# Kernel tuning notes

Hardware: AMD Instinct MI355X
Metric: run time of the kernel (lower is better)

Reference implementation:

```python
import jax, jax.numpy as jnp
import numpy as np

# ---- static config ----
G = 4          # num graphs
NG = 512       # nodes per graph
N = G * NG     # total nodes
E = 32768      # num edges
IN_DIM = 128
HID = 32
HEADS = 4
HC = HID * HEADS  # 128
OUT_DIM = 32
N_LAYERS = 2
GRID = 500
Q = 20
NEG_SLOPE = 0.2
QUANTILES = jnp.asarray(np.linspace(0.0, 1.0, Q), jnp.float32)  # [Q]


def setup_inputs() -> dict:
    key = jax.random.key(0)
    ks = jax.random.split(key, 32)
    inp = {}
    inp['x'] = jax.random.normal(ks[0], (N, IN_DIM), jnp.float32)
    inp['edge_index'] = jax.random.randint(ks[1], (2, E), 0, N).astype(jnp.int64)
    inp['batch'] = (jnp.arange(N) // NG).astype(jnp.int64)
    # GATConv params (2 layers, both 128 -> 4 heads x 32, concat)
    for l, (kin,) in enumerate([(IN_DIM,), (HC,)]):
        s = 1.0 / np.sqrt(kin)
        inp[f'W{l}'] = jax.random.normal(ks[2 + 4 * l], (kin, HC), jnp.float32) * s
        inp[f'as{l}'] = jax.random.normal(ks[3 + 4 * l], (HEADS, HID), jnp.float32) * s
        inp[f'ad{l}'] = jax.random.normal(ks[4 + 4 * l], (HEADS, HID), jnp.float32) * s
        inp[f'b{l}'] = jnp.zeros((HC,), jnp.float32)
    for l in range(N_LAYERS + 1):
        inp[f'lpW{l}'] = jax.random.normal(ks[10 + 2 * l], (HC, OUT_DIM), jnp.float32) * (1.0 / np.sqrt(HC))
        inp[f'lpb{l}'] = jnp.zeros((OUT_DIM,), jnp.float32)
    for l in range(N_LAYERS + 1):
        inp[f'kW{l}'] = jax.random.normal(ks[16 + 2 * l], (HC * Q, OUT_DIM), jnp.float32) * (1.0 / np.sqrt(HC * Q))
        inp[f'kb{l}'] = jnp.zeros((OUT_DIM,), jnp.float32)
    inp['pool_w'] = jnp.ones((2,), jnp.float32) / 2.0
    inp['beta'] = jax.random.normal(ks[22], (OUT_DIM,), jnp.float32)
    inp['h0'] = jax.random.normal(ks[23], (1,), jnp.float32)
    return inp


def _gat_layer(x, src, dst, W, a_src, a_dst, bias):
    # PyG GATConv (concat=True, add_self_loops=True, negative_slope=0.2), eval mode
    n = x.shape[0]
    xh = (x @ W).reshape(n, HEADS, HID)              # [N,H,C]
    loop = jnp.arange(n)
    s = jnp.concatenate([src, loop])                 # [E+N]
    d = jnp.concatenate([dst, loop])
    al_s = jnp.einsum('nhc,hc->nh', xh, a_src)       # [N,H]
    al_d = jnp.einsum('nhc,hc->nh', xh, a_dst)
    e = jax.nn.leaky_relu(al_s[s] + al_d[d], NEG_SLOPE)   # [E+N,H]
    e_max = jax.ops.segment_max(e, d, num_segments=n)     # stable softmax per dst
    e = jnp.exp(e - e_max[d])
    denom = jax.ops.segment_sum(e, d, num_segments=n)
    alpha = e / (denom[d] + 1e-16)                   # [E+N,H]
    out = jax.ops.segment_sum(alpha[:, :, None] * xh[s], d, num_segments=n)
    return out.reshape(n, HC) + bias


def _kde_per_graph(xg):
    # xg: [Ng, D] -> [D*Q] soft-quantile features via grid KDE
    n = xg.shape[0]
    mn = xg.min(axis=0) - 1e-6                       # [D]
    mx = xg.max(axis=0) + 1e-6
    grid = jnp.linspace(0.0, 1.0, GRID)[:, None] * (mx - mn) + mn   # [Gp,D]
    std = xg.std(axis=0) + 1e-8 / 3
    h = 1.06 * std * float(n) ** (-0.2)              # [D]
    u = (grid[:, None, :] - xg[None, :, :]) / h      # [Gp,Ng,D]  (dominant tensor)
    kern = jnp.exp(-0.5 * u * u) / (h * np.sqrt(2.0 * np.pi))
    density = kern.mean(axis=1)                      # [Gp,D]
    cdf = jnp.cumsum(density, axis=0)
    cdf = cdf / jnp.clip(cdf[-1:], 1e-8)
    dist = jnp.abs(cdf[:, :, None] - QUANTILES)      # [Gp,D,Q]
    w = jax.nn.sigmoid(-100.0 * dist)
    w = w / (w.sum(axis=0, keepdims=True) + 1e-8)
    qv = (grid[:, :, None] * w).sum(axis=0)          # [D,Q]
    return qv.reshape(-1)


def _readout(cur, lpW, lpb, kW, kb, pool_w):
    xr = cur.reshape(G, NG, -1)
    pooled = jnp.stack([xr.mean(axis=1), xr.max(axis=1)], axis=0)   # [2,G,D]
    wp = (pooled * pool_w[:, None, None]).sum(axis=0)               # [G,D]
    h = wp @ lpW + lpb                                              # [G,out]
    kf = jax.vmap(_kde_per_graph)(xr)                               # [G,D*Q]
    return h, kf @ kW + kb


def reference(x, edge_index, batch, W0, as0, ad0, b0, W1, as1, ad1, b1,
              lpW0, lpb0, lpW1, lpb1, lpW2, lpb2,
              kW0, kb0, kW1, kb1, kW2, kb2, pool_w, beta, h0):
    src, dst = edge_index[0], edge_index[1]
    convs = [(W0, as0, ad0, b0), (W1, as1, ad1, b1)]
    lps = [(lpW0, lpb0), (lpW1, lpb1), (lpW2, lpb2)]
    kps = [(kW0, kb0), (kW1, kb1), (kW2, kb2)]
    cur = x
    h_list, kde_list = [], []
    for i in range(N_LAYERS):
        h, kp = _readout(cur, lps[i][0], lps[i][1], kps[i][0], kps[i][1], pool_w)
        h_list.append(h); kde_list.append(kp)
        cur = _gat_layer(cur, src, dst, *convs[i])
        if i != N_LAYERS - 1:
            cur = jax.nn.relu(cur)
    h, kp = _readout(cur, lps[-1][0], lps[-1][1], kps[-1][0], kps[-1][1], pool_w)
    h_list.append(h); kde_list.append(kp)
    main_out = jnp.stack(h_list).mean(axis=0)        # [G,out]
    kde_out = jnp.stack(kde_list).mean(axis=0)
    risk = (main_out + kde_out) @ beta + h0          # [G]
    return risk
```

## Files before the change

### kernel.cpp

```cpp
#include <hip/hip_runtime.h>
#include <math.h>

#define GNUM 4
#define NG 512
#define NN 2048
#define EE 32768
#define HC 128
#define HEADS 4
#define HID 32
#define GRID_PTS 500
#define QN 20
#define ODIM 32
#define MAXE 160

#define LOG2E 1.44269504088896340736f
#define NEG_HALF_LOG2E -0.72134752044448170368f
#define N_POW_M02 0.2871745887492588f
#define SIG_K 144.269504089f

__device__ __forceinline__ float fexp2(float x){ return __builtin_amdgcn_exp2f(x); }
__device__ __forceinline__ float frcp(float x){ return __builtin_amdgcn_rcpf(x); }

struct SmemKDE {
  __align__(16) float2 xs[NG];
  float4 wred4[8];
  float sc[4];
  float wsum[8], woff[9];
  float redw[QN][8], redg[QN][8];
  float qs[QN];
};
struct SmemXW  { float rows[4][HC]; int cnt[4]; };
struct SmemGat {
  int   ssrc[4][MAXE];
  float sexp[4][MAXE][HEADS];
};
union Smem { SmemKDE kde; SmemXW xw; SmemGat gat; };

__device__ void kde_phase(Smem& sm, const float* __restrict__ cur, int do_relu, int trans,
        const float* __restrict__ kW, const float* __restrict__ kb, float* __restrict__ kacc,
        const float* __restrict__ lpW, const float* __restrict__ lpb,
        const float* __restrict__ poolw, float* __restrict__ macc){
  int b = blockIdx.x;
  int g = b >> 7, d = b & 127;
  int t = threadIdx.x;
  int lane = t & 63, wave = t >> 6;
  float v, v2;
  if (trans){
    float2 vv = ((const float2*)cur)[(size_t)d*NN + g*NG + t];
    v = vv.x; v2 = vv.y;
  } else {
    v = cur[((size_t)g*NG + t)*HC + d];
    v2 = v*v;
  }
  if (do_relu){ v = fmaxf(v, 0.f); v2 = v*v; }
  if (!trans) sm.kde.xs[t] = make_float2(v, v2);
  float mn=v, mx=v, smv=v, sq=v2;
  #pragma unroll
  for (int m=32; m>0; m>>=1){
    mn = fminf(mn, __shfl_xor(mn, m, 64));
    mx = fmaxf(mx, __shfl_xor(mx, m, 64));
    smv += __shfl_xor(smv, m, 64);
    sq += __shfl_xor(sq, m, 64);
  }
  if (lane==0) sm.kde.wred4[wave] = make_float4(mn,mx,smv,sq);
  __syncthreads();
  if (t==0){
    float4 r = sm.kde.wred4[0];
    #pragma unroll
    for (int i=1;i<8;++i){
      float4 bb = sm.kde.wred4[i];
      r.x = fminf(r.x,bb.x); r.y = fmaxf(r.y,bb.y); r.z += bb.z; r.w += bb.w;
    }
    float mean = r.z * (1.f/NG);
    float var  = fmaxf(r.w*(1.f/NG) - mean*mean, 0.f);
    float sd   = sqrtf(var) + (1e-8f/3.f);
    float h    = 1.06f * sd * N_POW_M02;
    float lo = r.x - 1e-6f, hi = r.y + 1e-6f;
    sm.kde.sc[0] = lo;
    sm.kde.sc[1] = (hi-lo)*(1.f/(GRID_PTS-1));
    sm.kde.sc[2] = NEG_HALF_LOG2E/(h*h);
    sm.kde.sc[3] = poolw[0]*mean + poolw[1]*r.y;
  }
  __syncthreads();
  float lo = sm.kde.sc[0], st = sm.kde.sc[1], kk = sm.kde.sc[2];
  float gv = lo + st*(float)t;
  float acc = 0.f;
  if (t < GRID_PTS){
    float c0 = kk*gv*gv, c1 = -2.f*kk*gv;
    const float4* p4 = trans ? ((const float4*)cur) + (((size_t)d*NN + g*NG) >> 1)
                             : (const float4*)sm.kde.xs;
    #pragma unroll 4
    for (int i=0;i<NG/2;++i){
      float4 s2 = p4[i];
      acc += fexp2(fmaf(kk, s2.y, fmaf(c1, s2.x, c0)));
      acc += fexp2(fmaf(kk, s2.w, fmaf(c1, s2.z, c0)));
    }
  }
  float sv = acc;
  #pragma unroll
  for (int off=1; off<64; off<<=1){
    float n = __shfl_up(sv, off, 64);
    if (lane >= off) sv += n;
  }
  if (lane==63) sm.kde.wsum[wave] = sv;
  __syncthreads();
  if (t==0){
    float r2 = 0.f;
    #pragma unroll
    for (int i=0;i<8;++i){ sm.kde.woff[i]=r2; r2+=sm.kde.wsum[i]; }
    sm.kde.woff[8]=r2;
  }
  if (t < QN*8){ ((float*)sm.kde.redw)[t]=0.f; ((float*)sm.kde.redg)[t]=0.f; }
  __syncthreads();
  float invt = 1.f/fmaxf(sm.kde.woff[8], 1e-8f);
  float c = (sv + sm.kde.woff[wave]) * invt;
  float cw0 = __shfl(c, 0, 64), cw1 = __shfl(c, 63, 64);
  int qlo = max(0, (int)ceilf((cw0 - 0.17f)*(float)(QN-1)));
  int qhi = min(QN-1, (int)floorf((cw1 + 0.17f)*(float)(QN-1)));
  for (int q=qlo; q<=qhi; ++q){
    float w = 0.f;
    if (t < GRID_PTS){
      float dist = fabsf(c - (float)q*(1.f/(QN-1)));
      w = frcp(1.f + fexp2(SIG_K*dist));
    }
    float gw = gv*w;
    #pragma unroll
    for (int m=32;m>0;m>>=1){
      w  += __shfl_xor(w,  m, 64);
      gw += __shfl_xor(gw, m, 64);
    }
    if (lane==0){ sm.kde.redw[q][wave]=w; sm.kde.redg[q][wave]=gw; }
  }
  __syncthreads();
  if (t < QN){
    float sw=0.f, sgw=0.f;
    #pragma unroll
    for (int i=0;i<8;++i){ sw+=sm.kde.redw[t][i]; sgw+=sm.kde.redg[t][i]; }
    sm.kde.qs[t] = sgw / (sw + 1e-8f);
  }
  __syncthreads();
  if (t < ODIM){
    float a = 0.f;
    const float* kwb = kW + (size_t)d*QN*ODIM + t;
    #pragma unroll
    for (int q=0;q<QN;++q) a += sm.kde.qs[q]*kwb[q*ODIM];
    if (d==0) a += kb[t];
    kacc[(size_t)d*128 + g*ODIM + t] = a;
    float bb = sm.kde.sc[3]*lpW[d*ODIM + t];
    if (d==0) bb += lpb[t];
    macc[(size_t)d*128 + g*ODIM + t] = bb;
  }
  __syncthreads();
}

__device__ float gather_core(Smem& sm, int d, int sub, int tl,
        const int* __restrict__ csr, const int* __restrict__ deg,
        const float* __restrict__ als, const float* __restrict__ ald,
        const float* __restrict__ xh, const float* __restrict__ bias){
  int dg = deg[d];
  int E = dg + 1;
  const int* base = csr + d*MAXE;
  float a0 = ald[d*4+0], a1 = ald[d*4+1], a2 = ald[d*4+2], a3 = ald[d*4+3];
  for (int i=tl; i<E; i+=128){
    int s = (i < dg) ? base[i] : d;
    sm.gat.ssrc[sub][i] = s;
    float e0 = als[s*4+0]+a0, e1 = als[s*4+1]+a1, e2 = als[s*4+2]+a2, e3 = als[s*4+3]+a3;
    e0 = (e0>=0.f)? e0 : 0.2f*e0;
    e1 = (e1>=0.f)? e1 : 0.2f*e1;
    e2 = (e2>=0.f)? e2 : 0.2f*e2;
    e3 = (e3>=0.f)? e3 : 0.2f*e3;
    sm.gat.sexp[sub][i][0]=e0; sm.gat.sexp[sub][i][1]=e1;
    sm.gat.sexp[sub][i][2]=e2; sm.gat.sexp[sub][i][3]=e3;
  }
  __syncthreads();
  int h = tl >> 5, l32 = tl & 31;
  float mx = -INFINITY;
  for (int i=l32; i<E; i+=32) mx = fmaxf(mx, sm.gat.sexp[sub][i][h]);
  #pragma unroll
  for (int m=16; m>0; m>>=1) mx = fmaxf(mx, __shfl_xor(mx, m, 32));
  float sdn = 0.f;
  for (int i=l32; i<E; i+=32){
    float ev = fexp2(LOG2E*(sm.gat.sexp[sub][i][h] - mx));
    sm.gat.sexp[sub][i][h] = ev;
    sdn += ev;
  }
  #pragma unroll
  for (int m=16; m>0; m>>=1) sdn += __shfl_xor(sdn, m, 32);
  float fac = 1.f/(sdn + 1e-16f);
  float acc = bias[tl];
  for (int i=0;i<E;++i)
    acc += sm.gat.sexp[sub][i][h]*fac * xh[(size_t)sm.gat.ssrc[sub][i]*HC + tl];
  __syncthreads();
  return acc;
}

__device__ void xw_emit(Smem& sm, int sub, int j, int n,
        const float* __restrict__ W, const float* __restrict__ as_, const float* __restrict__ ad_,
        float* __restrict__ xh, float* __restrict__ als, float* __restrict__ ald){
  float acc = 0.f;
  #pragma unroll 8
  for (int c2=0;c2<HC;++c2)
    acc += sm.xw.rows[sub][c2]*W[(size_t)c2*HC + j];
  xh[(size_t)n*HC + j] = acc;
  int h = j >> 5, cc = j & 31;
  float ps = acc*as_[h*HID+cc], pd = acc*ad_[h*HID+cc];
  #pragma unroll
  for (int m=16;m>0;m>>=1){
    ps += __shfl_xor(ps, m, 32);
    pd += __shfl_xor(pd, m, 32);
  }
  if (cc==0){ als[n*HEADS+h]=ps; ald[n*HEADS+h]=pd; }
}

__device__ void write_transposed(Smem& sm, int t, int n0, float* __restrict__ curT){
  if (t < HC){
    float v0 = sm.xw.rows[0][t], v1 = sm.xw.rows[1][t];
    float v2 = sm.xw.rows[2][t], v3 = sm.xw.rows[3][t];
    float4* p = (float4*)(curT + (((size_t)t*NN + n0) << 1));
    p[0] = make_float4(v0, v0*v0, v1, v1*v1);
    p[1] = make_float4(v2, v2*v2, v3, v3*v3);
  }
}

__global__ __launch_bounds__(512) void k_L0(const float* __restrict__ x,
        const float* __restrict__ kW, const float* __restrict__ kb, float* __restrict__ kacc,
        const float* __restrict__ lpW, const float* __restrict__ lpb,
        const float* __restrict__ poolw, float* __restrict__ macc,
        const float* __restrict__ W, const float* __restrict__ as_, const float* __restrict__ ad_,
        float* __restrict__ xh, float* __restrict__ als, float* __restrict__ ald,
        const int* __restrict__ src, const int* __restrict__ dst,
        int* __restrict__ deg, int* __restrict__ csr){
  __shared__ Smem sm;
  int t = threadIdx.x;
  if (blockIdx.x < 512){
    kde_phase(sm, x, 0, 0, kW, kb, kacc, lpW, lpb, poolw, macc);
  } else {
    int b2 = blockIdx.x - 512;
    int sub = t >> 7, j = t & 127;
    int n = b2*4 + sub;
    if (t < 4) sm.xw.cnt[t] = 0;
    sm.xw.rows[sub][j] = x[(size_t)n*HC + j];
    __syncthreads();
    int base4 = b2*4;
    for (int e = t; e < EE; e += 512){
      int dd = dst[e];
      unsigned r = (unsigned)(dd - base4);
      if (r < 4u){
        int p = atomicAdd(&sm.xw.cnt[r], 1);
        if (p < MAXE) csr[dd*MAXE + p] = src[e];
      }
    }
    xw_emit(sm, sub, j, n, W, as_, ad_, xh, als, ald);
    __syncthreads();
    if (t < 4) deg[base4 + t] = min(sm.xw.cnt[t], MAXE-1);
  }
}

__global__ __launch_bounds__(512) void k_G0(const int* __restrict__ csr, const int* __restrict__ deg,
        const float* __restrict__ als_in, const float* __restrict__ ald_in,
        const float* __restrict__ xh_in, const float* __restrict__ bias,
        float* __restrict__ cur1T,
        const float* __restrict__ W1, const float* __restrict__ as1, const float* __restrict__ ad1,
        float* __restrict__ xh2, float* __restrict__ als2, float* __restrict__ ald2){
  __shared__ Smem sm;
  int t = threadIdx.x;
  int sub = t >> 7, tl = t & 127;
  int d = blockIdx.x*4 + sub;
  float acc = gather_core(sm, d, sub, tl, csr, deg, als_in, ald_in, xh_in, bias);
  sm.xw.rows[sub][tl] = fmaxf(acc, 0.f);
  __syncthreads();
  write_transposed(sm, t, blockIdx.x*4, cur1T);
  xw_emit(sm, sub, tl, d, W1, as1, ad1, xh2, als2, ald2);
}

__global__ __launch_bounds__(512) void k_L1(const float* __restrict__ cur1T,
        const float* __restrict__ kW, const float* __restrict__ kb, float* __restrict__ kacc,
        const float* __restrict__ lpW, const float* __restrict__ lpb,
        const float* __restrict__ poolw, float* __restrict__ macc,
        const int* __restrict__ csr, const int* __restrict__ deg,
        const float* __restrict__ als2, const float* __restrict__ ald2,
        const float* __restrict__ xh2, const float* __restrict__ bias,
        float* __restrict__ cur2T){
  __shared__ Smem sm;
  int t = threadIdx.x;
  if (blockIdx.x < 512){
    kde_phase(sm, cur1T, 0, 1, kW, kb, kacc, lpW, lpb, poolw, macc);
  } else {
    int b2 = blockIdx.x - 512;
    int sub = t >> 7, tl = t & 127;
    int d = b2*4 + sub;
    float acc = gather_core(sm, d, sub, tl, csr, deg, als2, ald2, xh2, bias);
    sm.xw.rows[sub][tl] = acc;
    __syncthreads();
    write_transposed(sm, t, b2*4, cur2T);
  }
}

__global__ __launch_bounds__(512) void k_L2(const float* __restrict__ cur2T,
        const float* __restrict__ kW, const float* __restrict__ kb, float* __restrict__ kacc,
        const float* __restrict__ lpW, const float* __restrict__ lpb,
        const float* __restrict__ poolw, float* __restrict__ macc){
  __shared__ Smem sm;
  kde_phase(sm, cur2T, 0, 1, kW, kb, kacc, lpW, lpb, poolw, macc);
}

__global__ __launch_bounds__(384) void k_final(const float* __restrict__ mpart, const float* __restrict__ kpart,
                        const float* __restrict__ beta, const float* __restrict__ h0,
                        float* __restrict__ out){
  int t = threadIdx.x;
  __shared__ float sdm[384];
  int l = t >> 7, tt = t & 127;
  const float* mrow = mpart + (size_t)l*16384 + tt;
  const float* krow = kpart + (size_t)l*16384 + tt;
  float s = 0.f;
  #pragma unroll 8
  for (int d2=0; d2<128; ++d2) s += mrow[(size_t)d2*128] + krow[(size_t)d2*128];
  sdm[t] = s;
  __syncthreads();
  if (t < 128){
    int g = t >> 5, o = t & 31;
    float s3 = (sdm[t] + sdm[t+128] + sdm[t+256]) * (1.f/3.f) * beta[o];
    #pragma unroll
    for (int m=16; m>0; m>>=1) s3 += __shfl_xor(s3, m, 32);
    if (o == 0) out[g] = s3 + h0[0];
  }
}

extern "C" void kernel_launch(void* const* d_in, const int* in_sizes, int n_in,
                              void* d_out, int out_size, void* d_ws, size_t ws_size,
                              hipStream_t stream) {
  (void)in_sizes; (void)n_in; (void)out_size; (void)ws_size;
  const float* x    = (const float*)d_in[0];
  const int*   ei   = (const int*)d_in[1];
  const int*   srcp = ei;
  const int*   dstp = ei + EE;
  const float* W[2]   = {(const float*)d_in[3], (const float*)d_in[7]};
  const float* As[2]  = {(const float*)d_in[4], (const float*)d_in[8]};
  const float* Ad[2]  = {(const float*)d_in[5], (const float*)d_in[9]};
  const float* Bi[2]  = {(const float*)d_in[6], (const float*)d_in[10]};
  const float* lpW[3] = {(const float*)d_in[11], (const float*)d_in[13], (const float*)d_in[15]};
  const float* lpb[3] = {(const float*)d_in[12], (const float*)d_in[14], (const float*)d_in[16]};
  const float* kW[3]  = {(const float*)d_in[17], (const float*)d_in[19], (const float*)d_in[21]};
  const float* kb[3]  = {(const float*)d_in[18], (const float*)d_in[20], (const float*)d_in[22]};
  const float* poolw  = (const float*)d_in[23];
  const float* beta   = (const float*)d_in[24];
  const float* h0     = (const float*)d_in[25];
  float* out = (float*)d_out;

  float* ws = (float*)d_ws;
  float* cur1T = ws;
  float* cur2T = cur1T + 524288;
  float* xh    = cur2T + 524288;
  float* xh2   = xh + 262144;
  float* als   = xh2 + 262144;
  float* ald   = als + 8192;
  float* als2  = ald + 8192;
  float* ald2  = als2 + 8192;
  float* mpart = ald2 + 8192;
  float* kpart = mpart + 49152;
  int*   deg   = (int*)(kpart + 49152);
  int*   csr   = deg + 2048;

  k_L0<<<1024, 512, 0, stream>>>(x, kW[0], kb[0], kpart, lpW[0], lpb[0], poolw, mpart,
                                 W[0], As[0], Ad[0], xh, als, ald,
                                 srcp, dstp, deg, csr);
  k_G0<<<512, 512, 0, stream>>>(csr, deg, als, ald, xh, Bi[0], cur1T,
                                W[1], As[1], Ad[1], xh2, als2, ald2);
  k_L1<<<1024, 512, 0, stream>>>(cur1T, kW[1], kb[1], kpart+16384, lpW[1], lpb[1], poolw, mpart+16384,
                                 csr, deg, als2, ald2, xh2, Bi[1], cur2T);
  k_L2<<<512, 512, 0, stream>>>(cur2T, kW[2], kb[2], kpart+32768, lpW[2], lpb[2], poolw, mpart+32768);
  k_final<<<1, 384, 0, stream>>>(mpart, kpart, beta, h0, out);
}
```

Measured before the change: 208.6 us.

## Merge all phases into one cooperative persistent kernel with grid syncs

Replaces the five separate kernel launches with a single cooperative kernel of 512 blocks that runs every phase and separates them with grid-wide barriers. Each block now does both the KDE readout work and the GAT work of a former dual-role launch, and the order alternates by block parity to balance load. This removes launch gaps and tail effects between kernels. The cost is fewer blocks per phase (512 instead of 1024), extra grid-sync latency, and a requirement that all blocks stay co-resident. If the cooperative launch fails, the code falls back to five separate launches.

```diff
diff --git a/kernel.cpp b/kernel.cpp
--- a/kernel.cpp
+++ b/kernel.cpp
@@ -1,5 +1,8 @@
 #include <hip/hip_runtime.h>
+#include <hip/hip_cooperative_groups.h>
 #include <math.h>
+
+namespace cg = cooperative_groups;
 
 #define GNUM 4
 #define NG 512
@@ -36,11 +39,21 @@
 };
 union Smem { SmemKDE kde; SmemXW xw; SmemGat gat; };
 
-__device__ void kde_phase(Smem& sm, const float* __restrict__ cur, int do_relu, int trans,
+struct Params {
+  const float *x; const int *src, *dst;
+  const float *W0,*as0,*ad0,*b0, *W1,*as1,*ad1,*b1;
+  const float *lpW0,*lpb0,*lpW1,*lpb1,*lpW2,*lpb2;
+  const float *kW0,*kb0,*kW1,*kb1,*kW2,*kb2;
+  const float *poolw,*beta,*h0;
+  float *cur1T,*cur2T,*xh,*xh2,*als,*ald,*als2,*ald2,*mpart,*kpart;
+  int *deg,*csr;
+  float *out;
+};
+
+__device__ void kde_phase(Smem& sm, const float* __restrict__ cur, int do_relu, int trans, int b,
         const float* __restrict__ kW, const float* __restrict__ kb, float* __restrict__ kacc,
         const float* __restrict__ lpW, const float* __restrict__ lpb,
         const float* __restrict__ poolw, float* __restrict__ macc){
-  int b = blockIdx.x;
   int g = b >> 7, d = b & 127;
   int t = threadIdx.x;
   int lane = t & 63, wave = t >> 6;
@@ -222,109 +235,112 @@
   }
 }
 
-__global__ __launch_bounds__(512) void k_L0(const float* __restrict__ x,
-        const float* __restrict__ kW, const float* __restrict__ kb, float* __restrict__ kacc,
-        const float* __restrict__ lpW, const float* __restrict__ lpb,
-        const float* __restrict__ poolw, float* __restrict__ macc,
-        const float* __restrict__ W, const float* __restrict__ as_, const float* __restrict__ ad_,
-        float* __restrict__ xh, float* __restrict__ als, float* __restrict__ ald,
-        const int* __restrict__ src, const int* __restrict__ dst,
-        int* __restrict__ deg, int* __restrict__ csr){
-  __shared__ Smem sm;
-  int t = threadIdx.x;
-  if (blockIdx.x < 512){
-    kde_phase(sm, x, 0, 0, kW, kb, kacc, lpW, lpb, poolw, macc);
+__device__ void xw0_task(Smem& sm, const Params& p, int bid, int t){
+  int sub = t >> 7, j = t & 127;
+  int n = bid*4 + sub;
+  if (t < 4) sm.xw.cnt[t] = 0;
+  sm.xw.rows[sub][j] = p.x[(size_t)n*HC + j];
+  __syncthreads();
+  int base4 = bid*4;
+  for (int e = t; e < EE; e += 512){
+    int dd = p.dst[e];
+    unsigned r = (unsigned)(dd - base4);
+    if (r < 4u){
+      int pp = atomicAdd(&sm.xw.cnt[r], 1);
+      if (pp < MAXE) p.csr[dd*MAXE + pp] = p.src[e];
+    }
+  }
+  xw_emit(sm, sub, j, n, p.W0, p.as0, p.ad0, p.xh, p.als, p.ald);
+  __syncthreads();
+  if (t < 4) p.deg[base4 + t] = min(sm.xw.cnt[t], MAXE-1);
+  __syncthreads();
+}
+
+__device__ void gather1_task(Smem& sm, const Params& p, int bid, int t){
+  int sub = t >> 7, tl = t & 127;
+  int d = bid*4 + sub;
+  float acc = gather_core(sm, d, sub, tl, p.csr, p.deg, p.als2, p.ald2, p.xh2, p.b1);
+  sm.xw.rows[sub][tl] = acc;
+  __syncthreads();
+  write_transposed(sm, t, bid*4, p.cur2T);
+  __syncthreads();
+}
+
+__device__ void phaseA(Smem& sm, const Params& p, int bid, int t){
+  if (bid & 1){
+    xw0_task(sm, p, bid, t);
+    kde_phase(sm, p.x, 0, 0, bid, p.kW0, p.kb0, p.kpart, p.lpW0, p.lpb0, p.poolw, p.mpart);
   } else {
-    int b2 = blockIdx.x - 512;
-    int sub = t >> 7, j = t & 127;
-    int n = b2*4 + sub;
-    if (t < 4) sm.xw.cnt[t] = 0;
-    sm.xw.rows[sub][j] = x[(size_t)n*HC + j];
-    __syncthreads();
-    int base4 = b2*4;
-    for (int e = t; e < EE; e += 512){
-      int dd = dst[e];
-      unsigned r = (unsigned)(dd - base4);
-      if (r < 4u){
-        int p = atomicAdd(&sm.xw.cnt[r], 1);
-        if (p < MAXE) csr[dd*MAXE + p] = src[e];
-      }
-    }
-    xw_emit(sm, sub, j, n, W, as_, ad_, xh, als, ald);
-    __syncthreads();
-    if (t < 4) deg[base4 + t] = min(sm.xw.cnt[t], MAXE-1);
-  }
-}
-
-__global__ __launch_bounds__(512) void k_G0(const int* __restrict__ csr, const int* __restrict__ deg,
-        const float* __restrict__ als_in, const float* __restrict__ ald_in,
-        const float* __restrict__ xh_in, const float* __restrict__ bias,
-        float* __restrict__ cur1T,
-        const float* __restrict__ W1, const float* __restrict__ as1, const float* __restrict__ ad1,
-        float* __restrict__ xh2, float* __restrict__ als2, float* __restrict__ ald2){
-  __shared__ Smem sm;
-  int t = threadIdx.x;
+    kde_phase(sm, p.x, 0, 0, bid, p.kW0, p.kb0, p.kpart, p.lpW0, p.lpb0, p.poolw, p.mpart);
+    xw0_task(sm, p, bid, t);
+  }
+}
+
+__device__ void phaseB(Smem& sm, const Params& p, int bid, int t){
   int sub = t >> 7, tl = t & 127;
-  int d = blockIdx.x*4 + sub;
-  float acc = gather_core(sm, d, sub, tl, csr, deg, als_in, ald_in, xh_in, bias);
+  int d = bid*4 + sub;
+  float acc = gather_core(sm, d, sub, tl, p.csr, p.deg, p.als, p.ald, p.xh, p.b0);
   sm.xw.rows[sub][tl] = fmaxf(acc, 0.f);
   __syncthreads();
-  write_transposed(sm, t, blockIdx.x*4, cur1T);
-  xw_emit(sm, sub, tl, d, W1, as1, ad1, xh2, als2, ald2);
-}
-
-__global__ __launch_bounds__(512) void k_L1(const float* __restrict__ cur1T,
-        const float* __restrict__ kW, const float* __restrict__ kb, float* __restrict__ kacc,
-        const float* __restrict__ lpW, const float* __restrict__ lpb,
-        const float* __restrict__ poolw, float* __restrict__ macc,
-        const int* __restrict__ csr, const int* __restrict__ deg,
-        const float* __restrict__ als2, const float* __restrict__ ald2,
-        const float* __restrict__ xh2, const float* __restrict__ bias,
-        float* __restrict__ cur2T){
-  __shared__ Smem sm;
-  int t = threadIdx.x;
-  if (blockIdx.x < 512){
-    kde_phase(sm, cur1T, 0, 1, kW, kb, kacc, lpW, lpb, poolw, macc);
+  write_transposed(sm, t, bid*4, p.cur1T);
+  xw_emit(sm, sub, tl, d, p.W1, p.as1, p.ad1, p.xh2, p.als2, p.ald2);
+}
+
+__device__ void phaseC(Smem& sm, const Params& p, int bid, int t){
+  if (bid & 1){
+    gather1_task(sm, p, bid, t);
+    kde_phase(sm, p.cur1T, 0, 1, bid, p.kW1, p.kb1, p.kpart+16384, p.lpW1, p.lpb1, p.poolw, p.mpart+16384);
   } else {
-    int b2 = blockIdx.x - 512;
-    int sub = t >> 7, tl = t & 127;
-    int d = b2*4 + sub;
-    float acc = gather_core(sm, d, sub, tl, csr, deg, als2, ald2, xh2, bias);
-    sm.xw.rows[sub][tl] = acc;
-    __syncthreads();
-    write_transposed(sm, t, b2*4, cur2T);
-  }
-}
-
-__global__ __launch_bounds__(512) void k_L2(const float* __restrict__ cur2T,
-        const float* __restrict__ kW, const float* __restrict__ kb, float* __restrict__ kacc,
-        const float* __restrict__ lpW, const float* __restrict__ lpb,
-        const float* __restrict__ poolw, float* __restrict__ macc){
-  __shared__ Smem sm;
-  kde_phase(sm, cur2T, 0, 1, kW, kb, kacc, lpW, lpb, poolw, macc);
-}
-
-__global__ __launch_bounds__(384) void k_final(const float* __restrict__ mpart, const float* __restrict__ kpart,
-                        const float* __restrict__ beta, const float* __restrict__ h0,
-                        float* __restrict__ out){
-  int t = threadIdx.x;
-  __shared__ float sdm[384];
-  int l = t >> 7, tt = t & 127;
-  const float* mrow = mpart + (size_t)l*16384 + tt;
-  const float* krow = kpart + (size_t)l*16384 + tt;
-  float s = 0.f;
-  #pragma unroll 8
-  for (int d2=0; d2<128; ++d2) s += mrow[(size_t)d2*128] + krow[(size_t)d2*128];
-  sdm[t] = s;
+    kde_phase(sm, p.cur1T, 0, 1, bid, p.kW1, p.kb1, p.kpart+16384, p.lpW1, p.lpb1, p.poolw, p.mpart+16384);
+    gather1_task(sm, p, bid, t);
+  }
+}
+
+__device__ void phaseD(Smem& sm, const Params& p, int bid, int t){
+  kde_phase(sm, p.cur2T, 0, 1, bid, p.kW2, p.kb2, p.kpart+32768, p.lpW2, p.lpb2, p.poolw, p.mpart+32768);
+}
+
+__device__ void phaseE(Smem& sm, const Params& p, int t){
+  float* sdm = (float*)sm.kde.xs;
+  if (t < 384){
+    int l = t >> 7, tt = t & 127;
+    const float* mrow = p.mpart + (size_t)l*16384 + tt;
+    const float* krow = p.kpart + (size_t)l*16384 + tt;
+    float s = 0.f;
+    #pragma unroll 8
+    for (int d2=0; d2<128; ++d2) s += mrow[(size_t)d2*128] + krow[(size_t)d2*128];
+    sdm[t] = s;
+  }
   __syncthreads();
   if (t < 128){
     int g = t >> 5, o = t & 31;
-    float s3 = (sdm[t] + sdm[t+128] + sdm[t+256]) * (1.f/3.f) * beta[o];
+    float s3 = (sdm[t] + sdm[t+128] + sdm[t+256]) * (1.f/3.f) * p.beta[o];
     #pragma unroll
     for (int m=16; m>0; m>>=1) s3 += __shfl_xor(s3, m, 32);
-    if (o == 0) out[g] = s3 + h0[0];
-  }
-}
+    if (o == 0) p.out[g] = s3 + p.h0[0];
+  }
+}
+
+__global__ __launch_bounds__(512, 4) void k_all(Params p){
+  __shared__ Smem sm;
+  cg::grid_group grid = cg::this_grid();
+  int bid = blockIdx.x, t = threadIdx.x;
+  phaseA(sm, p, bid, t);
+  grid.sync();
+  phaseB(sm, p, bid, t);
+  grid.sync();
+  phaseC(sm, p, bid, t);
+  grid.sync();
+  phaseD(sm, p, bid, t);
+  grid.sync();
+  if (bid == 0) phaseE(sm, p, t);
+}
+
+__global__ __launch_bounds__(512, 4) void k_pA(Params p){ __shared__ Smem sm; phaseA(sm, p, blockIdx.x, threadIdx.x); }
+__global__ __launch_bounds__(512, 4) void k_pB(Params p){ __shared__ Smem sm; phaseB(sm, p, blockIdx.x, threadIdx.x); }
+__global__ __launch_bounds__(512, 4) void k_pC(Params p){ __shared__ Smem sm; phaseC(sm, p, blockIdx.x, threadIdx.x); }
+__global__ __launch_bounds__(512, 4) void k_pD(Params p){ __shared__ Smem sm; phaseD(sm, p, blockIdx.x, threadIdx.x); }
+__global__ __launch_bounds__(512, 4) void k_pE(Params p){ __shared__ Smem sm; if (blockIdx.x == 0) phaseE(sm, p, threadIdx.x); }
 
 extern "C" void kernel_launch(void* const* d_in, const int* in_sizes, int n_in,
                               void* d_out, int out_size, void* d_ws, size_t ws_size,
@@ -332,20 +348,6 @@
   (void)in_sizes; (void)n_in; (void)out_size; (void)ws_size;
   const float* x    = (const float*)d_in[0];
   const int*   ei   = (const int*)d_in[1];
-  const int*   srcp = ei;
-  const int*   dstp = ei + EE;
-  const float* W[2]   = {(const float*)d_in[3], (const float*)d_in[7]};
-  const float* As[2]  = {(const float*)d_in[4], (const float*)d_in[8]};
-  const float* Ad[2]  = {(const float*)d_in[5], (const float*)d_in[9]};
-  const float* Bi[2]  = {(const float*)d_in[6], (const float*)d_in[10]};
-  const float* lpW[3] = {(const float*)d_in[11], (const float*)d_in[13], (const float*)d_in[15]};
-  const float* lpb[3] = {(const float*)d_in[12], (const float*)d_in[14], (const float*)d_in[16]};
-  const float* kW[3]  = {(const float*)d_in[17], (const float*)d_in[19], (const float*)d_in[21]};
-  const float* kb[3]  = {(const float*)d_in[18], (const float*)d_in[20], (const float*)d_in[22]};
-  const float* poolw  = (const float*)d_in[23];
-  const float* beta   = (const float*)d_in[24];
-  const float* h0     = (const float*)d_in[25];
-  float* out = (float*)d_out;
 
   float* ws = (float*)d_ws;
   float* cur1T = ws;
@@ -361,13 +363,34 @@
   int*   deg   = (int*)(kpart + 49152);
   int*   csr   = deg + 2048;
 
-  k_L0<<<1024, 512, 0, stream>>>(x, kW[0], kb[0], kpart, lpW[0], lpb[0], poolw, mpart,
-                                 W[0], As[0], Ad[0], xh, als, ald,
-                                 srcp, dstp, deg, csr);
-  k_G0<<<512, 512, 0, stream>>>(csr, deg, als, ald, xh, Bi[0], cur1T,
-                                W[1], As[1], Ad[1], xh2, als2, ald2);
-  k_L1<<<1024, 512, 0, stream>>>(cur1T, kW[1], kb[1], kpart+16384, lpW[1], lpb[1], poolw, mpart+16384,
-                                 csr, deg, als2, ald2, xh2, Bi[1], cur2T);
-  k_L2<<<512, 512, 0, stream>>>(cur2T, kW[2], kb[2], kpart+32768, lpW[2], lpb[2], poolw, mpart+32768);
-  k_final<<<1, 384, 0, stream>>>(mpart, kpart, beta, h0, out);
-}
+  Params prm;
+  prm.x = x; prm.src = ei; prm.dst = ei + EE;
+  prm.W0 = (const float*)d_in[3];  prm.as0 = (const float*)d_in[4];
+  prm.ad0 = (const float*)d_in[5]; prm.b0  = (const float*)d_in[6];
+  prm.W1 = (const float*)d_in[7];  prm.as1 = (const float*)d_in[8];
+  prm.ad1 = (const float*)d_in[9]; prm.b1  = (const float*)d_in[10];
+  prm.lpW0 = (const float*)d_in[11]; prm.lpb0 = (const float*)d_in[12];
+  prm.lpW1 = (const float*)d_in[13]; prm.lpb1 = (const float*)d_in[14];
+  prm.lpW2 = (const float*)d_in[15]; prm.lpb2 = (const float*)d_in[16];
+  prm.kW0 = (const float*)d_in[17]; prm.kb0 = (const float*)d_in[18];
+  prm.kW1 = (const float*)d_in[19]; prm.kb1 = (const float*)d_in[20];
+  prm.kW2 = (const float*)d_in[21]; prm.kb2 = (const float*)d_in[22];
+  prm.poolw = (const float*)d_in[23];
+  prm.beta  = (const float*)d_in[24];
+  prm.h0    = (const float*)d_in[25];
+  prm.cur1T = cur1T; prm.cur2T = cur2T; prm.xh = xh; prm.xh2 = xh2;
+  prm.als = als; prm.ald = ald; prm.als2 = als2; prm.ald2 = ald2;
+  prm.mpart = mpart; prm.kpart = kpart; prm.deg = deg; prm.csr = csr;
+  prm.out = (float*)d_out;
+
+  void* kargs[] = { (void*)&prm };
+  hipError_t err = hipLaunchCooperativeKernel((const void*)k_all, dim3(512), dim3(512),
+                                              kargs, 0, stream);
+  if (err != hipSuccess){
+    k_pA<<<512, 512, 0, stream>>>(prm);
+    k_pB<<<512, 512, 0, stream>>>(prm);
+    k_pC<<<512, 512, 0, stream>>>(prm);
+    k_pD<<<512, 512, 0, stream>>>(prm);
+    k_pE<<<1,   512, 0, stream>>>(prm);
+  }
+}
```

New measurement: 498.8 us. 139% more time.

## Pretranspose input for KDE layer 0 and unroll GAT gather with padded edges

Applied to the files above, without the earlier changes.

Adds a small transpose kernel that writes x as interleaved (v, v^2) per feature column so the layer-0 KDE reads contiguous global data instead of strided loads and shared-memory staging. kde_phase is reduced to a single transposed path, and the grid-point guard becomes a post-loop mask so all threads run the loop uniformly. The GAT gather pads edge lists to a multiple of eight with zero weights and unrolls the weighted sum by eight to expose more memory-level parallelism. This costs an extra kernel launch and workspace buffer, plus wasted work on padded edges and threads past the grid range.

```diff
diff --git a/kernel.cpp b/kernel.cpp
--- a/kernel.cpp
+++ b/kernel.cpp
@@ -22,7 +22,6 @@
 __device__ __forceinline__ float frcp(float x){ return __builtin_amdgcn_rcpf(x); }
 
 struct SmemKDE {
-  __align__(16) float2 xs[NG];
   float4 wred4[8];
   float sc[4];
   float wsum[8], woff[9];
@@ -36,7 +35,7 @@
 };
 union Smem { SmemKDE kde; SmemXW xw; SmemGat gat; };
 
-__device__ void kde_phase(Smem& sm, const float* __restrict__ cur, int do_relu, int trans,
+__device__ void kde_phase(Smem& sm, const float* __restrict__ curT,
         const float* __restrict__ kW, const float* __restrict__ kb, float* __restrict__ kacc,
         const float* __restrict__ lpW, const float* __restrict__ lpb,
         const float* __restrict__ poolw, float* __restrict__ macc){
@@ -44,16 +43,8 @@
   int g = b >> 7, d = b & 127;
   int t = threadIdx.x;
   int lane = t & 63, wave = t >> 6;
-  float v, v2;
-  if (trans){
-    float2 vv = ((const float2*)cur)[(size_t)d*NN + g*NG + t];
-    v = vv.x; v2 = vv.y;
-  } else {
-    v = cur[((size_t)g*NG + t)*HC + d];
-    v2 = v*v;
-  }
-  if (do_relu){ v = fmaxf(v, 0.f); v2 = v*v; }
-  if (!trans) sm.kde.xs[t] = make_float2(v, v2);
+  float2 vv = ((const float2*)curT)[(size_t)d*NN + g*NG + t];
+  float v = vv.x, v2 = vv.y;
   float mn=v, mx=v, smv=v, sq=v2;
   #pragma unroll
   for (int m=32; m>0; m>>=1){
@@ -85,10 +76,9 @@
   float lo = sm.kde.sc[0], st = sm.kde.sc[1], kk = sm.kde.sc[2];
   float gv = lo + st*(float)t;
   float acc = 0.f;
-  if (t < GRID_PTS){
+  {
     float c0 = kk*gv*gv, c1 = -2.f*kk*gv;
-    const float4* p4 = trans ? ((const float4*)cur) + (((size_t)d*NN + g*NG) >> 1)
-                             : (const float4*)sm.kde.xs;
+    const float4* p4 = (const float4*)curT + (((size_t)d*NN + g*NG) >> 1);
     #pragma unroll 4
     for (int i=0;i<NG/2;++i){
       float4 s2 = p4[i];
@@ -96,6 +86,7 @@
       acc += fexp2(fmaf(kk, s2.w, fmaf(c1, s2.z, c0)));
     }
   }
+  if (t >= GRID_PTS) acc = 0.f;
   float sv = acc;
   #pragma unroll
   for (int off=1; off<64; off<<=1){
@@ -159,18 +150,24 @@
         const float* __restrict__ xh, const float* __restrict__ bias){
   int dg = deg[d];
   int E = dg + 1;
+  int Ep = (E + 7) & ~7;
   const int* base = csr + d*MAXE;
   float a0 = ald[d*4+0], a1 = ald[d*4+1], a2 = ald[d*4+2], a3 = ald[d*4+3];
-  for (int i=tl; i<E; i+=128){
+  for (int i=tl; i<Ep; i+=128){
     int s = (i < dg) ? base[i] : d;
     sm.gat.ssrc[sub][i] = s;
-    float e0 = als[s*4+0]+a0, e1 = als[s*4+1]+a1, e2 = als[s*4+2]+a2, e3 = als[s*4+3]+a3;
-    e0 = (e0>=0.f)? e0 : 0.2f*e0;
-    e1 = (e1>=0.f)? e1 : 0.2f*e1;
-    e2 = (e2>=0.f)? e2 : 0.2f*e2;
-    e3 = (e3>=0.f)? e3 : 0.2f*e3;
-    sm.gat.sexp[sub][i][0]=e0; sm.gat.sexp[sub][i][1]=e1;
-    sm.gat.sexp[sub][i][2]=e2; sm.gat.sexp[sub][i][3]=e3;
+    if (i < E){
+      float e0 = als[s*4+0]+a0, e1 = als[s*4+1]+a1, e2 = als[s*4+2]+a2, e3 = als[s*4+3]+a3;
+      e0 = (e0>=0.f)? e0 : 0.2f*e0;
+      e1 = (e1>=0.f)? e1 : 0.2f*e1;
+      e2 = (e2>=0.f)? e2 : 0.2f*e2;
+      e3 = (e3>=0.f)? e3 : 0.2f*e3;
+      sm.gat.sexp[sub][i][0]=e0; sm.gat.sexp[sub][i][1]=e1;
+      sm.gat.sexp[sub][i][2]=e2; sm.gat.sexp[sub][i][3]=e3;
+    } else {
+      sm.gat.sexp[sub][i][0]=0.f; sm.gat.sexp[sub][i][1]=0.f;
+      sm.gat.sexp[sub][i][2]=0.f; sm.gat.sexp[sub][i][3]=0.f;
+    }
   }
   __syncthreads();
   int h = tl >> 5, l32 = tl & 31;
@@ -188,8 +185,13 @@
   for (int m=16; m>0; m>>=1) sdn += __shfl_xor(sdn, m, 32);
   float fac = 1.f/(sdn + 1e-16f);
   float acc = bias[tl];
-  for (int i=0;i<E;++i)
-    acc += sm.gat.sexp[sub][i][h]*fac * xh[(size_t)sm.gat.ssrc[sub][i]*HC + tl];
+  for (int i0=0; i0<Ep; i0+=8){
+    #pragma unroll
+    for (int k=0;k<8;++k){
+      int i = i0 + k;
+      acc += sm.gat.sexp[sub][i][h]*fac * xh[(size_t)sm.gat.ssrc[sub][i]*HC + tl];
+    }
+  }
   __syncthreads();
   return acc;
 }
@@ -222,7 +224,22 @@
   }
 }
 
-__global__ __launch_bounds__(512) void k_L0(const float* __restrict__ x,
+__global__ __launch_bounds__(512) void k_T(const float* __restrict__ x, float* __restrict__ xT){
+  __shared__ float rows[4][HC];
+  int t = threadIdx.x;
+  int sub = t >> 7, j = t & 127;
+  int n0 = blockIdx.x*4;
+  rows[sub][j] = x[(size_t)(n0+sub)*HC + j];
+  __syncthreads();
+  if (t < HC){
+    float v0 = rows[0][t], v1 = rows[1][t], v2 = rows[2][t], v3 = rows[3][t];
+    float4* p = (float4*)(xT + (((size_t)t*NN + n0) << 1));
+    p[0] = make_float4(v0, v0*v0, v1, v1*v1);
+    p[1] = make_float4(v2, v2*v2, v3, v3*v3);
+  }
+}
+
+__global__ __launch_bounds__(512) void k_L0(const float* __restrict__ x, const float* __restrict__ xT,
         const float* __restrict__ kW, const float* __restrict__ kb, float* __restrict__ kacc,
         const float* __restrict__ lpW, const float* __restrict__ lpb,
         const float* __restrict__ poolw, float* __restrict__ macc,
@@ -233,7 +250,7 @@
   __shared__ Smem sm;
   int t = threadIdx.x;
   if (blockIdx.x < 512){
-    kde_phase(sm, x, 0, 0, kW, kb, kacc, lpW, lpb, poolw, macc);
+    kde_phase(sm, xT, kW, kb, kacc, lpW, lpb, poolw, macc);
   } else {
     int b2 = blockIdx.x - 512;
     int sub = t >> 7, j = t & 127;
@@ -284,7 +301,7 @@
   __shared__ Smem sm;
   int t = threadIdx.x;
   if (blockIdx.x < 512){
-    kde_phase(sm, cur1T, 0, 1, kW, kb, kacc, lpW, lpb, poolw, macc);
+    kde_phase(sm, cur1T, kW, kb, kacc, lpW, lpb, poolw, macc);
   } else {
     int b2 = blockIdx.x - 512;
     int sub = t >> 7, tl = t & 127;
@@ -301,7 +318,7 @@
         const float* __restrict__ lpW, const float* __restrict__ lpb,
         const float* __restrict__ poolw, float* __restrict__ macc){
   __shared__ Smem sm;
-  kde_phase(sm, cur2T, 0, 1, kW, kb, kacc, lpW, lpb, poolw, macc);
+  kde_phase(sm, cur2T, kW, kb, kacc, lpW, lpb, poolw, macc);
 }
 
 __global__ __launch_bounds__(384) void k_final(const float* __restrict__ mpart, const float* __restrict__ kpart,
@@ -350,7 +367,8 @@
   float* ws = (float*)d_ws;
   float* cur1T = ws;
   float* cur2T = cur1T + 524288;
-  float* xh    = cur2T + 524288;
+  float* xT    = cur2T + 524288;
+  float* xh    = xT + 524288;
   float* xh2   = xh + 262144;
   float* als   = xh2 + 262144;
   float* ald   = als + 8192;
@@ -361,7 +379,8 @@
   int*   deg   = (int*)(kpart + 49152);
   int*   csr   = deg + 2048;
 
-  k_L0<<<1024, 512, 0, stream>>>(x, kW[0], kb[0], kpart, lpW[0], lpb[0], poolw, mpart,
+  k_T<<<512, 512, 0, stream>>>(x, xT);
+  k_L0<<<1024, 512, 0, stream>>>(x, xT, kW[0], kb[0], kpart, lpW[0], lpb[0], poolw, mpart,
                                  W[0], As[0], Ad[0], xh, als, ald,
                                  srcp, dstp, deg, csr);
   k_G0<<<512, 512, 0, stream>>>(csr, deg, als, ald, xh, Bi[0], cur1T,
```

After: 214.1 us. +2.6%, slower.
